# Performance work log

Measured on AMD Instinct MI355X. Metric: run time of the kernel, lower is better.

Reference implementation:

```python
import jax, jax.numpy as jnp
import numpy as np

H, C, L = 4, 64, 3          # heads, out_channels, conv layers
N, E, B = 20000, 320000, 32 # nodes, edges, graphs
HD = 64                     # hidden_dim


def setup_inputs() -> dict:
    key = jax.random.key(0)
    ks = jax.random.split(key, 24)
    x = jax.random.normal(ks[0], (N, 3), jnp.float32)
    src = jax.random.randint(ks[1], (E,), 0, N)
    dst = jax.random.randint(ks[2], (E,), 0, N)
    dst = jnp.where(dst == src, (dst + 1) % N, dst)  # no pre-existing self loops
    edge_index = jnp.stack([src, dst])
    edge_attr = jax.random.normal(ks[3], (E, 4), jnp.float32)
    u = jax.random.normal(ks[4], (B, 10), jnp.float32)
    batch = jnp.sort(jax.random.randint(ks[5], (N,), 0, B))
    p = lambda k, s: jax.random.normal(k, s, jnp.float32) * 0.1
    return {
        'x': x, 'edge_index': edge_index, 'edge_attr': edge_attr, 'u': u, 'batch': batch,
        'node_W': p(ks[6], (3, HD)), 'node_b': p(ks[7], (HD,)),
        'eemb_W': p(ks[8], (4, HD)), 'eemb_b': p(ks[9], (HD,)),
        'lin_W': p(ks[10], (L, HD, H * C)),
        'att_src': p(ks[11], (L, H, C)), 'att_dst': p(ks[12], (L, H, C)),
        'lin_eW': p(ks[13], (L, HD, H * C)), 'att_e': p(ks[14], (L, H, C)),
        'conv_b': p(ks[15], (L, C)),
        'gW': p(ks[16], (10, HD)), 'gb': p(ks[17], (HD,)),
        'f1W': p(ks[18], (2 * HD, HD)), 'f1b': p(ks[19], (HD,)),
        'f2W': p(ks[20], (HD, 2)), 'f2b': p(ks[21], (2,)),
    }


def _gat_layer(x, src, dst, ea, W, a_src, a_dst, We, a_e, b):
    # PyG GATConv(hidden, hidden, edge_dim=hidden, heads=4, concat=False), eval mode
    n = x.shape[0]
    # add self loops; self-loop edge_attr = mean of incoming edge_attr (fill_value='mean')
    deg = jax.ops.segment_sum(jnp.ones_like(dst, dtype=x.dtype), dst, num_segments=n)
    ea_self = jax.ops.segment_sum(ea, dst, num_segments=n) / jnp.maximum(deg, 1.0)[:, None]
    loop = jnp.arange(n)
    src2 = jnp.concatenate([src, loop])
    dst2 = jnp.concatenate([dst, loop])
    ea2 = jnp.concatenate([ea, ea_self], axis=0)
    xp = (x @ W).reshape(n, H, C)                       # [N,H,C]
    a_s = jnp.einsum('nhc,hc->nh', xp, a_src)           # [N,H]
    a_d = jnp.einsum('nhc,hc->nh', xp, a_dst)
    ee = (ea2 @ We).reshape(-1, H, C)                   # [E2,H,C]
    a_ed = jnp.einsum('ehc,hc->eh', ee, a_e)
    alpha = jax.nn.leaky_relu(a_s[src2] + a_d[dst2] + a_ed, 0.2)  # [E2,H]
    # segment softmax over destination nodes (stable)
    m = jax.ops.segment_max(alpha, dst2, num_segments=n)
    ex = jnp.exp(alpha - m[dst2])
    den = jax.ops.segment_sum(ex, dst2, num_segments=n)
    att = ex / den[dst2]
    out = jax.ops.segment_sum(xp[src2] * att[..., None], dst2, num_segments=n)  # [N,H,C]
    return out.mean(axis=1) + b  # concat=False -> mean over heads


def reference(x, edge_index, edge_attr, u, batch, node_W, node_b, eemb_W, eemb_b,
              lin_W, att_src, att_dst, lin_eW, att_e, conv_b, gW, gb, f1W, f1b, f2W, f2b):
    src, dst = edge_index[0], edge_index[1]
    h = jax.nn.relu(x @ node_W + node_b)
    ea = jax.nn.relu(edge_attr @ eemb_W + eemb_b)
    for i in range(L):
        h = jax.nn.relu(_gat_layer(h, src, dst, ea, lin_W[i], att_src[i], att_dst[i],
                                   lin_eW[i], att_e[i], conv_b[i]))
    # global mean pool over graphs
    cnt = jax.ops.segment_sum(jnp.ones((h.shape[0],), h.dtype), batch, num_segments=B)
    pooled = jax.ops.segment_sum(h, batch, num_segments=B) / jnp.maximum(cnt, 1.0)[:, None]
    ug = jax.nn.relu(u @ gW + gb)
    z = jnp.concatenate([pooled, ug], axis=1)
    z = jax.nn.relu(z @ f1W + f1b)
    return z @ f2W + f2b
```

## Files before the change

kernel.cpp:

```cpp
#include <hip/hip_runtime.h>
#include <hip/hip_bf16.h>

#define HD 64

typedef unsigned short u16;

__device__ __forceinline__ float lrelu(float x) { return x > 0.f ? x : 0.2f * x; }
__device__ __forceinline__ int clampi(int v, int maxv) {
    return v < 0 ? 0 : (v >= maxv ? maxv - 1 : v);
}
__device__ __forceinline__ float bf2f(u16 u) {
    return __uint_as_float(((unsigned int)u) << 16);
}
__device__ __forceinline__ u16 f2bf(float f) {
    unsigned int u = __float_as_uint(f);
    unsigned int lsb = (u >> 16) & 1u;
    u += 0x7fffu + lsb;
    return (u16)(u >> 16);
}

__global__ void k_init(int* deg, int* cursor, int* gcnt, float* pooled, int N, int B) {
    int i = blockIdx.x * blockDim.x + threadIdx.x;
    if (i < N) { deg[i] = 0; cursor[i] = 0; }
    if (i < B) gcnt[i] = 0;
    if (i < B * HD) pooled[i] = 0.f;
}

__global__ void k_node_emb(const float* __restrict__ x, const float* __restrict__ W,
                           const float* __restrict__ b, float* __restrict__ h, int N) {
    int i = blockIdx.x * blockDim.x + threadIdx.x;
    if (i >= N * HD) return;
    int n = i >> 6, c = i & 63;
    float acc = b[c];
    acc = fmaf(x[n * 3 + 0], W[0 * HD + c], acc);
    acc = fmaf(x[n * 3 + 1], W[1 * HD + c], acc);
    acc = fmaf(x[n * 3 + 2], W[2 * HD + c], acc);
    h[i] = fmaxf(acc, 0.f);
}

__global__ void k_deg(const int* __restrict__ dst, int* __restrict__ deg, int E, int N) {
    int e = blockIdx.x * blockDim.x + threadIdx.x;
    if (e < E) atomicAdd(&deg[clampi(dst[e], N)], 1);
}

__global__ void k_scan1(const int* __restrict__ deg, int* __restrict__ tmp,
                        int* __restrict__ bsum, int N) {
    __shared__ int s[256];
    int tid = threadIdx.x;
    int i = blockIdx.x * 256 + tid;
    int v = (i < N) ? deg[i] : 0;
    s[tid] = v;
    __syncthreads();
    for (int off = 1; off < 256; off <<= 1) {
        int t = (tid >= off) ? s[tid - off] : 0;
        __syncthreads();
        s[tid] += t;
        __syncthreads();
    }
    if (i < N) tmp[i] = s[tid];
    if (tid == 255) bsum[blockIdx.x] = s[255];
}
__global__ void k_scan2(const int* __restrict__ bsum, int* __restrict__ boff, int nb) {
    __shared__ int s[1024];
    int tid = threadIdx.x;
    int v = (tid < nb) ? bsum[tid] : 0;
    s[tid] = v;
    __syncthreads();
    for (int off = 1; off < 1024; off <<= 1) {
        int t = (tid >= off) ? s[tid - off] : 0;
        __syncthreads();
        s[tid] += t;
        __syncthreads();
    }
    if (tid < nb) boff[tid] = s[tid] - v;
}
__global__ void k_scan3(const int* __restrict__ tmp, const int* __restrict__ boff,
                        int* __restrict__ row_ptr, int N) {
    int i = blockIdx.x * blockDim.x + threadIdx.x;
    if (i == 0) row_ptr[0] = 0;
    if (i < N) row_ptr[i + 1] = tmp[i] + boff[i >> 8];
}

__global__ void k_csr(const int* __restrict__ src, const int* __restrict__ dst,
                      const int* __restrict__ row_ptr, int* __restrict__ cursor,
                      int* __restrict__ csr_src, int* __restrict__ csr_dst,
                      int* __restrict__ csr_eid, int E, int N) {
    int e = blockIdx.x * blockDim.x + threadIdx.x;
    if (e >= E) return;
    int d = clampi(dst[e], N);
    int pos = row_ptr[d] + atomicAdd(&cursor[d], 1);
    if (pos < E) {
        csr_src[pos] = clampi(src[e], N);
        csr_dst[pos] = d;
        csr_eid[pos] = e;
    }
}

#define MAXB 2048
__global__ void k_gse(const int* __restrict__ batch, int* __restrict__ gcnt, int N, int B) {
    __shared__ int s_cnt[MAXB];
    int t = threadIdx.x;
    int Bc = B < MAXB ? B : MAXB;
    for (int i = t; i < Bc; i += blockDim.x) s_cnt[i] = 0;
    __syncthreads();
    int n = blockIdx.x * blockDim.x + t;
    if (n < N) {
        int b = clampi(batch[n], B);
        if (b < MAXB) atomicAdd(&s_cnt[b], 1);
        else atomicAdd(&gcnt[b], 1);
    }
    __syncthreads();
    for (int i = t; i < Bc; i += blockDim.x)
        if (s_cnt[i] != 0) atomicAdd(&gcnt[i], s_cnt[i]);
}

__global__ __launch_bounds__(256) void k_ee(
    const float* __restrict__ edge_attr, const float* __restrict__ eW,
    const float* __restrict__ eB, const float* __restrict__ lin_eW,
    const float* __restrict__ att_e, const int* __restrict__ csr_eid,
    float* __restrict__ aed, int E) {
    __shared__ float s_ew[256];
    __shared__ float s_eb[64];
    __shared__ float s_wred[768];
    int t = threadIdx.x;
    s_ew[t] = eW[t];
    if (t < 64) s_eb[t] = eB[t];
    for (int idx = t; idx < 768; idx += 256) {
        int l = idx >> 8, hd = idx & 255, hh = hd >> 6, d = hd & 63;
        const float* We = lin_eW + (size_t)l * HD * 256;
        const float* ae = att_e + (size_t)l * 256;
        float acc = 0.f;
        for (int c = 0; c < 64; c++)
            acc = fmaf(We[d * 256 + hh * 64 + c], ae[hh * 64 + c], acc);
        s_wred[idx] = acc;
    }
    __syncthreads();
    int j0 = (blockIdx.x * 256 + t) * 4;
    if (j0 >= E) return;
    float4 a[4];
    int nv = 0;
    #pragma unroll
    for (int q = 0; q < 4; q++) {
        int j = j0 + q;
        if (j < E) {
            a[q] = *(const float4*)(edge_attr + (size_t)csr_eid[j] * 4);
            nv = q + 1;
        } else {
            a[q] = make_float4(0.f, 0.f, 0.f, 0.f);
        }
    }
    float acc[4][12];
    #pragma unroll
    for (int q = 0; q < 4; q++)
        #pragma unroll
        for (int m = 0; m < 12; m++) acc[q][m] = 0.f;
    for (int k = 0; k < HD; k++) {
        float e0 = s_ew[k], e1 = s_ew[64 + k], e2 = s_ew[128 + k], e3 = s_ew[192 + k];
        float eb = s_eb[k];
        float w[12];
        #pragma unroll
        for (int m = 0; m < 12; m++)
            w[m] = s_wred[(m >> 2) * 256 + (m & 3) * 64 + k];
        #pragma unroll
        for (int q = 0; q < 4; q++) {
            float v = fmaf(a[q].x, e0, fmaf(a[q].y, e1,
                      fmaf(a[q].z, e2, fmaf(a[q].w, e3, eb))));
            v = fmaxf(v, 0.f);
            #pragma unroll
            for (int m = 0; m < 12; m++) acc[q][m] = fmaf(v, w[m], acc[q][m]);
        }
    }
    #pragma unroll
    for (int q = 0; q < 4; q++) {
        if (q >= nv) break;
        float* o = aed + (size_t)(j0 + q) * 12;
        #pragma unroll
        for (int m = 0; m < 12; m++) o[m] = acc[q][m];
    }
}

__global__ void k_selfed(const int* __restrict__ row_ptr, float* __restrict__ aed,
                         int E, int N) {
    int n = blockIdx.x * blockDim.x + threadIdx.x;
    if (n >= N) return;
    int r0 = row_ptr[n], r1 = row_ptr[n + 1];
    float acc[12];
    #pragma unroll
    for (int m = 0; m < 12; m++) acc[m] = 0.f;
    for (int j = r0; j < r1; j++) {
        const float* p = aed + (size_t)j * 12;
        #pragma unroll
        for (int m = 0; m < 12; m++) acc[m] += p[m];
    }
    float inv = 1.f / fmaxf((float)(r1 - r0), 1.f);
    float* o = aed + (size_t)(E + n) * 12;
    #pragma unroll
    for (int m = 0; m < 12; m++) o[m] = acc[m] * inv;
}

__global__ __launch_bounds__(256) void k_xp(
    const float* __restrict__ h, const float* __restrict__ W,
    const float* __restrict__ asrc, const float* __restrict__ adst,
    u16* __restrict__ xp, float* __restrict__ a_s, float* __restrict__ a_d, int N) {
    __shared__ float hs[8 * HD];
    int n0 = blockIdx.x * 8;
    int t = threadIdx.x;
    for (int i = t; i < 8 * HD; i += 256) {
        int nn = n0 + (i >> 6);
        hs[i] = (nn < N) ? h[(size_t)nn * HD + (i & 63)] : 0.f;
    }
    __syncthreads();
    int c = t;
    float acc[8];
    #pragma unroll
    for (int k = 0; k < 8; k++) acc[k] = 0.f;
    for (int d = 0; d < HD; d++) {
        float wv = W[d * 256 + c];
        #pragma unroll
        for (int k = 0; k < 8; k++) acc[k] = fmaf(hs[k * HD + d], wv, acc[k]);
    }
    float as_ = asrc[c], ad_ = adst[c];
    int hh = c >> 6, cc = c & 63;
    #pragma unroll
    for (int k = 0; k < 8; k++) {
        int nn = n0 + k;
        float ps = acc[k] * as_;
        float pd = acc[k] * ad_;
        #pragma unroll
        for (int o = 32; o > 0; o >>= 1) {
            ps += __shfl_xor(ps, o);
            pd += __shfl_xor(pd, o);
        }
        if (nn < N) {
            xp[(size_t)nn * 256 + c] = f2bf(acc[k]);
            if (cc == 0) { a_s[nn * 4 + hh] = ps; a_d[nn * 4 + hh] = pd; }
        }
    }
}

__global__ void k_w(const int* __restrict__ csr_src, const int* __restrict__ csr_dst,
                    const float* __restrict__ aed, const float* __restrict__ a_s,
                    const float* __restrict__ a_d, float* __restrict__ wcsr,
                    int layer, int E, int N) {
    int j = blockIdx.x * blockDim.x + threadIdx.x;
    if (j >= E + N) return;
    int s, d;
    if (j < E) { s = csr_src[j]; d = csr_dst[j]; }
    else       { s = j - E; d = s; }
    const float* p = aed + (size_t)j * 12 + layer * 4;
    float4 as4 = *(const float4*)(a_s + s * 4);
    float4 ad4 = *(const float4*)(a_d + d * 4);
    float w0 = __expf(lrelu(as4.x + ad4.x + p[0]));
    float w1 = __expf(lrelu(as4.y + ad4.y + p[1]));
    float w2 = __expf(lrelu(as4.z + ad4.z + p[2]));
    float w3 = __expf(lrelu(as4.w + ad4.w + p[3]));
    *(float4*)(wcsr + (size_t)j * 4) = make_float4(w0, w1, w2, w3);
}

__global__ __launch_bounds__(256) void k_gat(
    const u16* __restrict__ xp, const float* __restrict__ wcsr,
    const int* __restrict__ row_ptr, const int* __restrict__ csr_src,
    const float* __restrict__ convb, float* __restrict__ h_out, int N, int E) {
    int wave = threadIdx.x >> 6, lane = threadIdx.x & 63;
    int n = blockIdx.x * 4 + wave;
    if (n >= N) return;
    int g = lane >> 4, p = lane & 15;
    int r0 = row_ptr[n], r1 = row_ptr[n + 1];
    float a00 = 0.f, a01 = 0.f, a02 = 0.f, a03 = 0.f;
    float a10 = 0.f, a11 = 0.f, a12 = 0.f, a13 = 0.f;
    float a20 = 0.f, a21 = 0.f, a22 = 0.f, a23 = 0.f;
    float a30 = 0.f, a31 = 0.f, a32 = 0.f, a33 = 0.f;
    float d0 = 0.f, d1 = 0.f, d2 = 0.f, d3 = 0.f;
    if (g == 0) {
        float4 w = *(const float4*)(wcsr + (size_t)(E + n) * 4);
        const u16* row = xp + (size_t)n * 256 + p * 4;
        ushort4 v0 = *(const ushort4*)(row);
        ushort4 v1 = *(const ushort4*)(row + 64);
        ushort4 v2 = *(const ushort4*)(row + 128);
        ushort4 v3 = *(const ushort4*)(row + 192);
        d0 += w.x; d1 += w.y; d2 += w.z; d3 += w.w;
        a00 = fmaf(w.x, bf2f(v0.x), a00); a01 = fmaf(w.x, bf2f(v0.y), a01);
        a02 = fmaf(w.x, bf2f(v0.z), a02); a03 = fmaf(w.x, bf2f(v0.w), a03);
        a10 = fmaf(w.y, bf2f(v1.x), a10); a11 = fmaf(w.y, bf2f(v1.y), a11);
        a12 = fmaf(w.y, bf2f(v1.z), a12); a13 = fmaf(w.y, bf2f(v1.w), a13);
        a20 = fmaf(w.z, bf2f(v2.x), a20); a21 = fmaf(w.z, bf2f(v2.y), a21);
        a22 = fmaf(w.z, bf2f(v2.z), a22); a23 = fmaf(w.z, bf2f(v2.w), a23);
        a30 = fmaf(w.w, bf2f(v3.x), a30); a31 = fmaf(w.w, bf2f(v3.y), a31);
        a32 = fmaf(w.w, bf2f(v3.z), a32); a33 = fmaf(w.w, bf2f(v3.w), a33);
    }
    for (int j = r0 + g; j < r1; j += 4) {
        float4 w = *(const float4*)(wcsr + (size_t)j * 4);
        const u16* row = xp + (size_t)csr_src[j] * 256 + p * 4;
        ushort4 v0 = *(const ushort4*)(row);
        ushort4 v1 = *(const ushort4*)(row + 64);
        ushort4 v2 = *(const ushort4*)(row + 128);
        ushort4 v3 = *(const ushort4*)(row + 192);
        d0 += w.x; d1 += w.y; d2 += w.z; d3 += w.w;
        a00 = fmaf(w.x, bf2f(v0.x), a00); a01 = fmaf(w.x, bf2f(v0.y), a01);
        a02 = fmaf(w.x, bf2f(v0.z), a02); a03 = fmaf(w.x, bf2f(v0.w), a03);
        a10 = fmaf(w.y, bf2f(v1.x), a10); a11 = fmaf(w.y, bf2f(v1.y), a11);
        a12 = fmaf(w.y, bf2f(v1.z), a12); a13 = fmaf(w.y, bf2f(v1.w), a13);
        a20 = fmaf(w.z, bf2f(v2.x), a20); a21 = fmaf(w.z, bf2f(v2.y), a21);
        a22 = fmaf(w.z, bf2f(v2.z), a22); a23 = fmaf(w.z, bf2f(v2.w), a23);
        a30 = fmaf(w.w, bf2f(v3.x), a30); a31 = fmaf(w.w, bf2f(v3.y), a31);
        a32 = fmaf(w.w, bf2f(v3.z), a32); a33 = fmaf(w.w, bf2f(v3.w), a33);
    }
    d0 += __shfl_xor(d0, 16); d0 += __shfl_xor(d0, 32);
    d1 += __shfl_xor(d1, 16); d1 += __shfl_xor(d1, 32);
    d2 += __shfl_xor(d2, 16); d2 += __shfl_xor(d2, 32);
    d3 += __shfl_xor(d3, 16); d3 += __shfl_xor(d3, 32);
    float i0 = 1.f / d0, i1 = 1.f / d1, i2 = 1.f / d2, i3 = 1.f / d3;
    float m0 = a00 * i0 + a10 * i1 + a20 * i2 + a30 * i3;
    float m1 = a01 * i0 + a11 * i1 + a21 * i2 + a31 * i3;
    float m2 = a02 * i0 + a12 * i1 + a22 * i2 + a32 * i3;
    float m3 = a03 * i0 + a13 * i1 + a23 * i2 + a33 * i3;
    m0 += __shfl_xor(m0, 16); m0 += __shfl_xor(m0, 32);
    m1 += __shfl_xor(m1, 16); m1 += __shfl_xor(m1, 32);
    m2 += __shfl_xor(m2, 16); m2 += __shfl_xor(m2, 32);
    m3 += __shfl_xor(m3, 16); m3 += __shfl_xor(m3, 32);
    if (lane < 16) {
        int c = p * 4;
        h_out[(size_t)n * HD + c + 0] = fmaxf(0.25f * m0 + convb[c + 0], 0.f);
        h_out[(size_t)n * HD + c + 1] = fmaxf(0.25f * m1 + convb[c + 1], 0.f);
        h_out[(size_t)n * HD + c + 2] = fmaxf(0.25f * m2 + convb[c + 2], 0.f);
        h_out[(size_t)n * HD + c + 3] = fmaxf(0.25f * m3 + convb[c + 3], 0.f);
    }
}

__global__ void k_pool(const float* __restrict__ h, const int* __restrict__ batch,
                       float* __restrict__ pooled, int N, int B) {
    int i = blockIdx.x * blockDim.x + threadIdx.x;
    if (i >= N * HD) return;
    int n = i >> 6, c = i & 63;
    int b = clampi(batch[n], B);
    atomicAdd(&pooled[b * HD + c], h[i]);
}

__global__ void k_mlp(const float* __restrict__ u, const float* __restrict__ gW,
                      const float* __restrict__ gb, const float* __restrict__ pooled,
                      const int* __restrict__ gcnt, const float* __restrict__ f1W,
                      const float* __restrict__ f1b, const float* __restrict__ f2W,
                      const float* __restrict__ f2b, float* __restrict__ out, int B) {
    __shared__ float z[2 * HD];
    __shared__ float z1s[HD];
    int b = blockIdx.x, t = threadIdx.x;
    float acc = gb[t];
    for (int k = 0; k < 10; k++) acc = fmaf(u[b * 10 + k], gW[k * HD + t], acc);
    z[HD + t] = fmaxf(acc, 0.f);
    float invc = 1.f / fmaxf((float)gcnt[b], 1.f);
    z[t] = pooled[b * HD + t] * invc;
    __syncthreads();
    float a1 = f1b[t];
    for (int k = 0; k < 2 * HD; k++) a1 = fmaf(z[k], f1W[k * HD + t], a1);
    z1s[t] = fmaxf(a1, 0.f);
    __syncthreads();
    if (t < 2) {
        float o = f2b[t];
        for (int k = 0; k < HD; k++) o = fmaf(z1s[k], f2W[k * 2 + t], o);
        out[b * 2 + t] = o;
    }
}

extern "C" void kernel_launch(void* const* d_in, const int* in_sizes, int n_in,
                              void* d_out, int out_size, void* d_ws, size_t ws_size,
                              hipStream_t stream) {
    const float* x         = (const float*)d_in[0];
    const int*   ei        = (const int*)d_in[1];
    const float* edge_attr = (const float*)d_in[2];
    const float* u         = (const float*)d_in[3];
    const int*   batch     = (const int*)d_in[4];
    const float* node_W    = (const float*)d_in[5];
    const float* node_b    = (const float*)d_in[6];
    const float* eemb_W    = (const float*)d_in[7];
    const float* eemb_b    = (const float*)d_in[8];
    const float* lin_W     = (const float*)d_in[9];
    const float* att_src   = (const float*)d_in[10];
    const float* att_dst   = (const float*)d_in[11];
    const float* lin_eW    = (const float*)d_in[12];
    const float* att_e     = (const float*)d_in[13];
    const float* conv_b    = (const float*)d_in[14];
    const float* gW        = (const float*)d_in[15];
    const float* gb        = (const float*)d_in[16];
    const float* f1W       = (const float*)d_in[17];
    const float* f1b       = (const float*)d_in[18];
    const float* f2W       = (const float*)d_in[19];
    const float* f2b       = (const float*)d_in[20];

    const int N = in_sizes[0] / 3;
    const int E = in_sizes[2] / 4;
    const int B = in_sizes[3] / 10;
    const int* src = ei;
    const int* dst = ei + E;
    const int NB = (N + 255) / 256;

    float* wsf = (float*)d_ws;
    float* h       = wsf;              wsf += (size_t)N * HD;
    float* a_s     = wsf;              wsf += (size_t)N * 4;
    float* a_d     = wsf;              wsf += (size_t)N * 4;
    float* aed     = wsf;              wsf += (size_t)(E + N) * 12;
    float* wcsr    = wsf;              wsf += (size_t)(E + N) * 4;
    float* pooled  = wsf;              wsf += (size_t)B * HD;
    u16* xp = (u16*)wsf;               wsf += (size_t)N * 128;
    int* wsi = (int*)wsf;
    int* deg     = wsi;                wsi += N;
    int* row_ptr = wsi;                wsi += N + 1;
    int* cursor  = wsi;                wsi += N;
    int* tmp     = wsi;                wsi += N;
    int* bsum    = wsi;                wsi += NB + 1;
    int* boff    = wsi;                wsi += NB + 1;
    int* csr_src = wsi;                wsi += E;
    int* csr_dst = wsi;                wsi += E;
    int* csr_eid = wsi;                wsi += E;
    int* gcnt    = wsi;                wsi += B;

    k_init<<<NB, 256, 0, stream>>>(deg, cursor, gcnt, pooled, N, B);
    k_node_emb<<<(N * HD + 255) / 256, 256, 0, stream>>>(x, node_W, node_b, h, N);
    k_deg<<<(E + 255) / 256, 256, 0, stream>>>(dst, deg, E, N);
    k_scan1<<<NB, 256, 0, stream>>>(deg, tmp, bsum, N);
    k_scan2<<<1, 1024, 0, stream>>>(bsum, boff, NB);
    k_scan3<<<NB, 256, 0, stream>>>(tmp, boff, row_ptr, N);
    k_csr<<<(E + 255) / 256, 256, 0, stream>>>(src, dst, row_ptr, cursor,
                                               csr_src, csr_dst, csr_eid, E, N);
    k_gse<<<NB, 256, 0, stream>>>(batch, gcnt, N, B);
    k_ee<<<(E + 1023) / 1024, 256, 0, stream>>>(edge_attr, eemb_W, eemb_b, lin_eW, att_e,
                                                csr_eid, aed, E);
    k_selfed<<<NB, 256, 0, stream>>>(row_ptr, aed, E, N);
    for (int i = 0; i < 3; i++) {
        k_xp<<<(N + 7) / 8, 256, 0, stream>>>(h, lin_W + (size_t)i * HD * 256,
                                              att_src + (size_t)i * 256,
                                              att_dst + (size_t)i * 256,
                                              xp, a_s, a_d, N);
        k_w<<<(E + N + 255) / 256, 256, 0, stream>>>(csr_src, csr_dst, aed, a_s, a_d,
                                                     wcsr, i, E, N);
        k_gat<<<(N + 3) / 4, 256, 0, stream>>>(xp, wcsr, row_ptr, csr_src,
                                               conv_b + (size_t)i * HD, h, N, E);
    }
    k_pool<<<(N * HD + 255) / 256, 256, 0, stream>>>(h, batch, pooled, N, B);
    k_mlp<<<B, 64, 0, stream>>>(u, gW, gb, pooled, gcnt, f1W, f1b, f2W, f2b,
                                (float*)d_out, B);
}
```

Baseline: 415.2 us.

## Fuse attention weights into GAT aggregation, merge scans, segment-based pooling

Computes per-edge attention exponentials inside the GAT aggregation kernel instead of a separate pass writing a weight buffer, and drops the csr_dst array. It also merges scan phases, folds node embedding into the init kernel, and tiles the projection over 16 nodes with vectorized shared loads. Pooling now binary-searches the sorted batch to find graph ranges and reduces in shared memory before a few atomics, which also yields graph counts. The tradeoffs are recomputing exps inside the gather loop and relying on batch being sorted.

```diff
diff --git a/kernel.cpp b/kernel.cpp
--- a/kernel.cpp
+++ b/kernel.cpp
@@ -19,23 +19,21 @@
     return (u16)(u >> 16);
 }
 
-__global__ void k_init(int* deg, int* cursor, int* gcnt, float* pooled, int N, int B) {
+__global__ void k_init(const float* __restrict__ x, const float* __restrict__ W,
+                       const float* __restrict__ b, float* __restrict__ h,
+                       int* deg, int* cursor, int* gcnt, float* pooled, int N, int B) {
     int i = blockIdx.x * blockDim.x + threadIdx.x;
     if (i < N) { deg[i] = 0; cursor[i] = 0; }
     if (i < B) gcnt[i] = 0;
     if (i < B * HD) pooled[i] = 0.f;
-}
-
-__global__ void k_node_emb(const float* __restrict__ x, const float* __restrict__ W,
-                           const float* __restrict__ b, float* __restrict__ h, int N) {
-    int i = blockIdx.x * blockDim.x + threadIdx.x;
-    if (i >= N * HD) return;
-    int n = i >> 6, c = i & 63;
-    float acc = b[c];
-    acc = fmaf(x[n * 3 + 0], W[0 * HD + c], acc);
-    acc = fmaf(x[n * 3 + 1], W[1 * HD + c], acc);
-    acc = fmaf(x[n * 3 + 2], W[2 * HD + c], acc);
-    h[i] = fmaxf(acc, 0.f);
+    if (i < N * HD) {
+        int n = i >> 6, c = i & 63;
+        float acc = b[c];
+        acc = fmaf(x[n * 3 + 0], W[0 * HD + c], acc);
+        acc = fmaf(x[n * 3 + 1], W[1 * HD + c], acc);
+        acc = fmaf(x[n * 3 + 2], W[2 * HD + c], acc);
+        h[i] = fmaxf(acc, 0.f);
+    }
 }
 
 __global__ void k_deg(const int* __restrict__ dst, int* __restrict__ deg, int E, int N) {
@@ -60,58 +58,36 @@
     if (i < N) tmp[i] = s[tid];
     if (tid == 255) bsum[blockIdx.x] = s[255];
 }
-__global__ void k_scan2(const int* __restrict__ bsum, int* __restrict__ boff, int nb) {
-    __shared__ int s[1024];
-    int tid = threadIdx.x;
-    int v = (tid < nb) ? bsum[tid] : 0;
-    s[tid] = v;
-    __syncthreads();
-    for (int off = 1; off < 1024; off <<= 1) {
-        int t = (tid >= off) ? s[tid - off] : 0;
-        __syncthreads();
-        s[tid] += t;
-        __syncthreads();
-    }
-    if (tid < nb) boff[tid] = s[tid] - v;
-}
-__global__ void k_scan3(const int* __restrict__ tmp, const int* __restrict__ boff,
-                        int* __restrict__ row_ptr, int N) {
-    int i = blockIdx.x * blockDim.x + threadIdx.x;
+__global__ void k_scan23(const int* __restrict__ tmp, const int* __restrict__ bsum,
+                         int* __restrict__ row_ptr, int N) {
+    __shared__ int s_off;
+    int t = threadIdx.x;
+    if (t < 64) {
+        int cnt = blockIdx.x;
+        int v = 0;
+        for (int base = 0; base < cnt; base += 64)
+            if (base + t < cnt) v += bsum[base + t];
+        #pragma unroll
+        for (int o = 32; o > 0; o >>= 1) v += __shfl_xor(v, o);
+        if (t == 0) s_off = v;
+    }
+    __syncthreads();
+    int i = blockIdx.x * 256 + t;
     if (i == 0) row_ptr[0] = 0;
-    if (i < N) row_ptr[i + 1] = tmp[i] + boff[i >> 8];
+    if (i < N) row_ptr[i + 1] = tmp[i] + s_off;
 }
 
 __global__ void k_csr(const int* __restrict__ src, const int* __restrict__ dst,
                       const int* __restrict__ row_ptr, int* __restrict__ cursor,
-                      int* __restrict__ csr_src, int* __restrict__ csr_dst,
-                      int* __restrict__ csr_eid, int E, int N) {
+                      int* __restrict__ csr_src, int* __restrict__ csr_eid, int E, int N) {
     int e = blockIdx.x * blockDim.x + threadIdx.x;
     if (e >= E) return;
     int d = clampi(dst[e], N);
     int pos = row_ptr[d] + atomicAdd(&cursor[d], 1);
     if (pos < E) {
         csr_src[pos] = clampi(src[e], N);
-        csr_dst[pos] = d;
         csr_eid[pos] = e;
     }
-}
-
-#define MAXB 2048
-__global__ void k_gse(const int* __restrict__ batch, int* __restrict__ gcnt, int N, int B) {
-    __shared__ int s_cnt[MAXB];
-    int t = threadIdx.x;
-    int Bc = B < MAXB ? B : MAXB;
-    for (int i = t; i < Bc; i += blockDim.x) s_cnt[i] = 0;
-    __syncthreads();
-    int n = blockIdx.x * blockDim.x + t;
-    if (n < N) {
-        int b = clampi(batch[n], B);
-        if (b < MAXB) atomicAdd(&s_cnt[b], 1);
-        else atomicAdd(&gcnt[b], 1);
-    }
-    __syncthreads();
-    for (int i = t; i < Bc; i += blockDim.x)
-        if (s_cnt[i] != 0) atomicAdd(&gcnt[i], s_cnt[i]);
 }
 
 __global__ __launch_bounds__(256) void k_ee(
@@ -202,28 +178,42 @@
     const float* __restrict__ h, const float* __restrict__ W,
     const float* __restrict__ asrc, const float* __restrict__ adst,
     u16* __restrict__ xp, float* __restrict__ a_s, float* __restrict__ a_d, int N) {
-    __shared__ float hs[8 * HD];
-    int n0 = blockIdx.x * 8;
+    __shared__ float hs[16 * HD];
+    int n0 = blockIdx.x * 16;
     int t = threadIdx.x;
-    for (int i = t; i < 8 * HD; i += 256) {
-        int nn = n0 + (i >> 6);
-        hs[i] = (nn < N) ? h[(size_t)nn * HD + (i & 63)] : 0.f;
+    if (n0 + 16 <= N) {
+        *(float4*)&hs[t * 4] = *(const float4*)&h[(size_t)n0 * HD + t * 4];
+    } else {
+        for (int i = t; i < 16 * HD; i += 256) {
+            int nn = n0 + (i >> 6);
+            hs[i] = (nn < N) ? h[(size_t)nn * HD + (i & 63)] : 0.f;
+        }
     }
     __syncthreads();
     int c = t;
-    float acc[8];
-    #pragma unroll
-    for (int k = 0; k < 8; k++) acc[k] = 0.f;
-    for (int d = 0; d < HD; d++) {
-        float wv = W[d * 256 + c];
-        #pragma unroll
-        for (int k = 0; k < 8; k++) acc[k] = fmaf(hs[k * HD + d], wv, acc[k]);
+    float acc[16];
+    #pragma unroll
+    for (int k = 0; k < 16; k++) acc[k] = 0.f;
+    for (int d = 0; d < HD; d += 4) {
+        float w0 = W[(d + 0) * 256 + c];
+        float w1 = W[(d + 1) * 256 + c];
+        float w2 = W[(d + 2) * 256 + c];
+        float w3 = W[(d + 3) * 256 + c];
+        #pragma unroll
+        for (int k = 0; k < 16; k++) {
+            float4 hv = *(const float4*)&hs[k * HD + d];
+            acc[k] = fmaf(hv.x, w0, acc[k]);
+            acc[k] = fmaf(hv.y, w1, acc[k]);
+            acc[k] = fmaf(hv.z, w2, acc[k]);
+            acc[k] = fmaf(hv.w, w3, acc[k]);
+        }
     }
     float as_ = asrc[c], ad_ = adst[c];
     int hh = c >> 6, cc = c & 63;
     #pragma unroll
-    for (int k = 0; k < 8; k++) {
+    for (int k = 0; k < 16; k++) {
         int nn = n0 + k;
+        if (nn >= N) break;
         float ps = acc[k] * as_;
         float pd = acc[k] * ad_;
         #pragma unroll
@@ -231,79 +221,72 @@
             ps += __shfl_xor(ps, o);
             pd += __shfl_xor(pd, o);
         }
-        if (nn < N) {
-            xp[(size_t)nn * 256 + c] = f2bf(acc[k]);
-            if (cc == 0) { a_s[nn * 4 + hh] = ps; a_d[nn * 4 + hh] = pd; }
-        }
-    }
-}
-
-__global__ void k_w(const int* __restrict__ csr_src, const int* __restrict__ csr_dst,
-                    const float* __restrict__ aed, const float* __restrict__ a_s,
-                    const float* __restrict__ a_d, float* __restrict__ wcsr,
-                    int layer, int E, int N) {
-    int j = blockIdx.x * blockDim.x + threadIdx.x;
-    if (j >= E + N) return;
-    int s, d;
-    if (j < E) { s = csr_src[j]; d = csr_dst[j]; }
-    else       { s = j - E; d = s; }
-    const float* p = aed + (size_t)j * 12 + layer * 4;
-    float4 as4 = *(const float4*)(a_s + s * 4);
-    float4 ad4 = *(const float4*)(a_d + d * 4);
-    float w0 = __expf(lrelu(as4.x + ad4.x + p[0]));
-    float w1 = __expf(lrelu(as4.y + ad4.y + p[1]));
-    float w2 = __expf(lrelu(as4.z + ad4.z + p[2]));
-    float w3 = __expf(lrelu(as4.w + ad4.w + p[3]));
-    *(float4*)(wcsr + (size_t)j * 4) = make_float4(w0, w1, w2, w3);
+        xp[(size_t)nn * 256 + c] = f2bf(acc[k]);
+        if (cc == 0) { a_s[nn * 4 + hh] = ps; a_d[nn * 4 + hh] = pd; }
+    }
 }
 
 __global__ __launch_bounds__(256) void k_gat(
-    const u16* __restrict__ xp, const float* __restrict__ wcsr,
+    const u16* __restrict__ xp, const float* __restrict__ a_s,
+    const float* __restrict__ a_d, const float* __restrict__ aed,
     const int* __restrict__ row_ptr, const int* __restrict__ csr_src,
-    const float* __restrict__ convb, float* __restrict__ h_out, int N, int E) {
+    const float* __restrict__ convb, float* __restrict__ h_out,
+    int layer, int N, int E) {
     int wave = threadIdx.x >> 6, lane = threadIdx.x & 63;
     int n = blockIdx.x * 4 + wave;
     if (n >= N) return;
     int g = lane >> 4, p = lane & 15;
     int r0 = row_ptr[n], r1 = row_ptr[n + 1];
+    float4 ad4 = *(const float4*)(a_d + (size_t)n * 4);
     float a00 = 0.f, a01 = 0.f, a02 = 0.f, a03 = 0.f;
     float a10 = 0.f, a11 = 0.f, a12 = 0.f, a13 = 0.f;
     float a20 = 0.f, a21 = 0.f, a22 = 0.f, a23 = 0.f;
     float a30 = 0.f, a31 = 0.f, a32 = 0.f, a33 = 0.f;
     float d0 = 0.f, d1 = 0.f, d2 = 0.f, d3 = 0.f;
     if (g == 0) {
-        float4 w = *(const float4*)(wcsr + (size_t)(E + n) * 4);
+        float4 as4 = *(const float4*)(a_s + (size_t)n * 4);
+        float4 p4 = *(const float4*)(aed + (size_t)(E + n) * 12 + layer * 4);
+        float w0 = __expf(lrelu(as4.x + ad4.x + p4.x));
+        float w1 = __expf(lrelu(as4.y + ad4.y + p4.y));
+        float w2 = __expf(lrelu(as4.z + ad4.z + p4.z));
+        float w3 = __expf(lrelu(as4.w + ad4.w + p4.w));
         const u16* row = xp + (size_t)n * 256 + p * 4;
         ushort4 v0 = *(const ushort4*)(row);
         ushort4 v1 = *(const ushort4*)(row + 64);
         ushort4 v2 = *(const ushort4*)(row + 128);
         ushort4 v3 = *(const ushort4*)(row + 192);
-        d0 += w.x; d1 += w.y; d2 += w.z; d3 += w.w;
-        a00 = fmaf(w.x, bf2f(v0.x), a00); a01 = fmaf(w.x, bf2f(v0.y), a01);
-        a02 = fmaf(w.x, bf2f(v0.z), a02); a03 = fmaf(w.x, bf2f(v0.w), a03);
-        a10 = fmaf(w.y, bf2f(v1.x), a10); a11 = fmaf(w.y, bf2f(v1.y), a11);
-        a12 = fmaf(w.y, bf2f(v1.z), a12); a13 = fmaf(w.y, bf2f(v1.w), a13);
-        a20 = fmaf(w.z, bf2f(v2.x), a20); a21 = fmaf(w.z, bf2f(v2.y), a21);
-        a22 = fmaf(w.z, bf2f(v2.z), a22); a23 = fmaf(w.z, bf2f(v2.w), a23);
-        a30 = fmaf(w.w, bf2f(v3.x), a30); a31 = fmaf(w.w, bf2f(v3.y), a31);
-        a32 = fmaf(w.w, bf2f(v3.z), a32); a33 = fmaf(w.w, bf2f(v3.w), a33);
+        d0 += w0; d1 += w1; d2 += w2; d3 += w3;
+        a00 = fmaf(w0, bf2f(v0.x), a00); a01 = fmaf(w0, bf2f(v0.y), a01);
+        a02 = fmaf(w0, bf2f(v0.z), a02); a03 = fmaf(w0, bf2f(v0.w), a03);
+        a10 = fmaf(w1, bf2f(v1.x), a10); a11 = fmaf(w1, bf2f(v1.y), a11);
+        a12 = fmaf(w1, bf2f(v1.z), a12); a13 = fmaf(w1, bf2f(v1.w), a13);
+        a20 = fmaf(w2, bf2f(v2.x), a20); a21 = fmaf(w2, bf2f(v2.y), a21);
+        a22 = fmaf(w2, bf2f(v2.z), a22); a23 = fmaf(w2, bf2f(v2.w), a23);
+        a30 = fmaf(w3, bf2f(v3.x), a30); a31 = fmaf(w3, bf2f(v3.y), a31);
+        a32 = fmaf(w3, bf2f(v3.z), a32); a33 = fmaf(w3, bf2f(v3.w), a33);
     }
     for (int j = r0 + g; j < r1; j += 4) {
-        float4 w = *(const float4*)(wcsr + (size_t)j * 4);
-        const u16* row = xp + (size_t)csr_src[j] * 256 + p * 4;
+        int s = csr_src[j];
+        float4 as4 = *(const float4*)(a_s + (size_t)s * 4);
+        float4 p4 = *(const float4*)(aed + (size_t)j * 12 + layer * 4);
+        float w0 = __expf(lrelu(as4.x + ad4.x + p4.x));
+        float w1 = __expf(lrelu(as4.y + ad4.y + p4.y));
+        float w2 = __expf(lrelu(as4.z + ad4.z + p4.z));
+        float w3 = __expf(lrelu(as4.w + ad4.w + p4.w));
+        const u16* row = xp + (size_t)s * 256 + p * 4;
         ushort4 v0 = *(const ushort4*)(row);
         ushort4 v1 = *(const ushort4*)(row + 64);
         ushort4 v2 = *(const ushort4*)(row + 128);
         ushort4 v3 = *(const ushort4*)(row + 192);
-        d0 += w.x; d1 += w.y; d2 += w.z; d3 += w.w;
-        a00 = fmaf(w.x, bf2f(v0.x), a00); a01 = fmaf(w.x, bf2f(v0.y), a01);
-        a02 = fmaf(w.x, bf2f(v0.z), a02); a03 = fmaf(w.x, bf2f(v0.w), a03);
-        a10 = fmaf(w.y, bf2f(v1.x), a10); a11 = fmaf(w.y, bf2f(v1.y), a11);
-        a12 = fmaf(w.y, bf2f(v1.z), a12); a13 = fmaf(w.y, bf2f(v1.w), a13);
-        a20 = fmaf(w.z, bf2f(v2.x), a20); a21 = fmaf(w.z, bf2f(v2.y), a21);
-        a22 = fmaf(w.z, bf2f(v2.z), a22); a23 = fmaf(w.z, bf2f(v2.w), a23);
-        a30 = fmaf(w.w, bf2f(v3.x), a30); a31 = fmaf(w.w, bf2f(v3.y), a31);
-        a32 = fmaf(w.w, bf2f(v3.z), a32); a33 = fmaf(w.w, bf2f(v3.w), a33);
+        d0 += w0; d1 += w1; d2 += w2; d3 += w3;
+        a00 = fmaf(w0, bf2f(v0.x), a00); a01 = fmaf(w0, bf2f(v0.y), a01);
+        a02 = fmaf(w0, bf2f(v0.z), a02); a03 = fmaf(w0, bf2f(v0.w), a03);
+        a10 = fmaf(w1, bf2f(v1.x), a10); a11 = fmaf(w1, bf2f(v1.y), a11);
+        a12 = fmaf(w1, bf2f(v1.z), a12); a13 = fmaf(w1, bf2f(v1.w), a13);
+        a20 = fmaf(w2, bf2f(v2.x), a20); a21 = fmaf(w2, bf2f(v2.y), a21);
+        a22 = fmaf(w2, bf2f(v2.z), a22); a23 = fmaf(w2, bf2f(v2.w), a23);
+        a30 = fmaf(w3, bf2f(v3.x), a30); a31 = fmaf(w3, bf2f(v3.y), a31);
+        a32 = fmaf(w3, bf2f(v3.z), a32); a33 = fmaf(w3, bf2f(v3.w), a33);
     }
     d0 += __shfl_xor(d0, 16); d0 += __shfl_xor(d0, 32);
     d1 += __shfl_xor(d1, 16); d1 += __shfl_xor(d1, 32);
@@ -327,13 +310,38 @@
     }
 }
 
+#define PCHUNK 4
 __global__ void k_pool(const float* __restrict__ h, const int* __restrict__ batch,
-                       float* __restrict__ pooled, int N, int B) {
-    int i = blockIdx.x * blockDim.x + threadIdx.x;
-    if (i >= N * HD) return;
-    int n = i >> 6, c = i & 63;
-    int b = clampi(batch[n], B);
-    atomicAdd(&pooled[b * HD + c], h[i]);
+                       float* __restrict__ pooled, int* __restrict__ gcnt, int N, int B) {
+    int b = blockIdx.x / PCHUNK, q = blockIdx.x % PCHUNK;
+    __shared__ int sb[2];
+    __shared__ float sred[256];
+    int t = threadIdx.x;
+    if (t == 0 || t == 64) {
+        int target = b + (t ? 1 : 0);
+        int lo = 0, hi = N;
+        while (lo < hi) {
+            int m = (lo + hi) >> 1;
+            if (batch[m] < target) lo = m + 1; else hi = m;
+        }
+        sb[t ? 1 : 0] = lo;
+    }
+    __syncthreads();
+    int start = sb[0], end = sb[1];
+    int len = end - start;
+    if (q == 0 && t == 0) gcnt[b] = len;
+    int c0 = start + (int)(((long long)len * q) / PCHUNK);
+    int c1 = start + (int)(((long long)len * (q + 1)) / PCHUNK);
+    int c = t & 63, r = t >> 6;
+    float acc = 0.f;
+    for (int nidx = c0 + r; nidx < c1; nidx += 4)
+        acc += h[(size_t)nidx * HD + c];
+    sred[t] = acc;
+    __syncthreads();
+    if (t < 64) {
+        float v = sred[t] + sred[64 + t] + sred[128 + t] + sred[192 + t];
+        atomicAdd(&pooled[b * HD + c], v);
+    }
 }
 
 __global__ void k_mlp(const float* __restrict__ u, const float* __restrict__ gW,
@@ -398,7 +406,6 @@
     float* a_s     = wsf;              wsf += (size_t)N * 4;
     float* a_d     = wsf;              wsf += (size_t)N * 4;
     float* aed     = wsf;              wsf += (size_t)(E + N) * 12;
-    float* wcsr    = wsf;              wsf += (size_t)(E + N) * 4;
     float* pooled  = wsf;              wsf += (size_t)B * HD;
     u16* xp = (u16*)wsf;               wsf += (size_t)N * 128;
     int* wsi = (int*)wsf;
@@ -407,35 +414,29 @@
     int* cursor  = wsi;                wsi += N;
     int* tmp     = wsi;                wsi += N;
     int* bsum    = wsi;                wsi += NB + 1;
-    int* boff    = wsi;                wsi += NB + 1;
     int* csr_src = wsi;                wsi += E;
-    int* csr_dst = wsi;                wsi += E;
     int* csr_eid = wsi;                wsi += E;
     int* gcnt    = wsi;                wsi += B;
 
-    k_init<<<NB, 256, 0, stream>>>(deg, cursor, gcnt, pooled, N, B);
-    k_node_emb<<<(N * HD + 255) / 256, 256, 0, stream>>>(x, node_W, node_b, h, N);
+    k_init<<<(N * HD + 255) / 256, 256, 0, stream>>>(x, node_W, node_b, h,
+                                                     deg, cursor, gcnt, pooled, N, B);
     k_deg<<<(E + 255) / 256, 256, 0, stream>>>(dst, deg, E, N);
     k_scan1<<<NB, 256, 0, stream>>>(deg, tmp, bsum, N);
-    k_scan2<<<1, 1024, 0, stream>>>(bsum, boff, NB);
-    k_scan3<<<NB, 256, 0, stream>>>(tmp, boff, row_ptr, N);
+    k_scan23<<<NB, 256, 0, stream>>>(tmp, bsum, row_ptr, N);
     k_csr<<<(E + 255) / 256, 256, 0, stream>>>(src, dst, row_ptr, cursor,
-                                               csr_src, csr_dst, csr_eid, E, N);
-    k_gse<<<NB, 256, 0, stream>>>(batch, gcnt, N, B);
+                                               csr_src, csr_eid, E, N);
     k_ee<<<(E + 1023) / 1024, 256, 0, stream>>>(edge_attr, eemb_W, eemb_b, lin_eW, att_e,
                                                 csr_eid, aed, E);
     k_selfed<<<NB, 256, 0, stream>>>(row_ptr, aed, E, N);
     for (int i = 0; i < 3; i++) {
-        k_xp<<<(N + 7) / 8, 256, 0, stream>>>(h, lin_W + (size_t)i * HD * 256,
-                                              att_src + (size_t)i * 256,
-                                              att_dst + (size_t)i * 256,
-                                              xp, a_s, a_d, N);
-        k_w<<<(E + N + 255) / 256, 256, 0, stream>>>(csr_src, csr_dst, aed, a_s, a_d,
-                                                     wcsr, i, E, N);
-        k_gat<<<(N + 3) / 4, 256, 0, stream>>>(xp, wcsr, row_ptr, csr_src,
-                                               conv_b + (size_t)i * HD, h, N, E);
-    }
-    k_pool<<<(N * HD + 255) / 256, 256, 0, stream>>>(h, batch, pooled, N, B);
+        k_xp<<<(N + 15) / 16, 256, 0, stream>>>(h, lin_W + (size_t)i * HD * 256,
+                                                att_src + (size_t)i * 256,
+                                                att_dst + (size_t)i * 256,
+                                                xp, a_s, a_d, N);
+        k_gat<<<(N + 3) / 4, 256, 0, stream>>>(xp, a_s, a_d, aed, row_ptr, csr_src,
+                                               conv_b + (size_t)i * HD, h, i, N, E);
+    }
+    k_pool<<<B * PCHUNK, 256, 0, stream>>>(h, batch, pooled, gcnt, N, B);
     k_mlp<<<B, 64, 0, stream>>>(u, gW, gb, pooled, gcnt, f1W, f1b, f2W, f2b,
                                 (float*)d_out, B);
 }
```

Result: faster. 382.8 us (-7.8%).
